# Performance work log

Hardware: AMD Instinct MI355X
Metric: run time of the kernel (lower is better)

## Reference

```python
import jax, jax.numpy as jnp
import numpy as np

N = 2048            # num nodes
AVG_DEG = 16
E0 = N * AVG_DEG    # random edges; self-loops appended -> E = E0 + N
IN_FEATS = 256
H = 16              # num_heads
HS = 32             # hidden_size (forced by linear001 = Linear(32,16))
D = HS // H         # head_dim = 2
EPS = 1e-5


def gat_conv(x, src, dst, W, al, ar, b):
    # DGL-style GATConv: x [N,F] -> [N,H,D]
    feat = (x @ W).reshape(N, H, D)                      # [N,H,D]
    el = (feat * al[None]).sum(-1)                       # [N,H] (src term)
    er = (feat * ar[None]).sum(-1)                       # [N,H] (dst term)
    e = jax.nn.leaky_relu(el[src] + er[dst], 0.2)        # [E,H]
    m = jax.ops.segment_max(e, dst, num_segments=N)      # segment softmax over incoming edges
    ex = jnp.exp(e - m[dst])
    s = jax.ops.segment_sum(ex, dst, num_segments=N)
    alpha = ex / s[dst]                                  # [E,H]
    out = jax.ops.segment_sum(alpha[:, :, None] * feat[src], dst, num_segments=N)
    return out + b.reshape(1, H, D)


def setup_inputs() -> dict:
    key = jax.random.key(0)
    ks = jax.random.split(key, 40)
    rn = lambda k, s, sc=0.1: (jax.random.normal(k, s, jnp.float32) * sc)
    loops = jnp.arange(N, dtype=jnp.int32)
    src = jnp.concatenate([jax.random.randint(ks[0], (E0,), 0, N, jnp.int32), loops])
    dst = jnp.concatenate([jax.random.randint(ks[1], (E0,), 0, N, jnp.int32), loops])
    inp = {
        'features': jax.random.normal(ks[2], (N, IN_FEATS), jnp.float32),
        'src': src, 'dst': dst,
        # GATConv 1
        'W1': rn(ks[3], (IN_FEATS, HS)), 'al1': rn(ks[4], (H, D)), 'ar1': rn(ks[5], (H, D)), 'bg1': rn(ks[6], (HS,)),
        # GATConv 2
        'W2': rn(ks[7], (HS, HS)), 'al2': rn(ks[8], (H, D)), 'ar2': rn(ks[9], (H, D)), 'bg2': rn(ks[10], (HS,)),
        # dense MHA projections
        'qw': rn(ks[11], (HS, HS)), 'qb': rn(ks[12], (HS,)),
        'kw': rn(ks[13], (HS, HS)), 'kb': rn(ks[14], (HS,)),
        'vw': rn(ks[15], (HS, HS)), 'vb': rn(ks[16], (HS,)),
        'ow': rn(ks[17], (HS, HS)), 'ob': rn(ks[18], (HS,)),
        # batchnorm affine
        'bn_g': jnp.ones((HS,), jnp.float32), 'bn_b': jnp.zeros((HS,), jnp.float32),
        # mlp
        'm1w': rn(ks[19], (HS, HS // 2)), 'm1b': rn(ks[20], (HS // 2,)),
        'm2w': rn(ks[21], (HS // 2, HS)), 'm2b': rn(ks[22], (HS,)),
        # scoring head
        'w001': rn(ks[23], (32, 16)), 'b001': rn(ks[24], (16,)),
        'w01': rn(ks[25], (16, 8)), 'b01': rn(ks[26], (8,)),
        'w1': rn(ks[27], (8, 4)), 'b1': rn(ks[28], (4,)),
        'w2': rn(ks[29], (4, 1)), 'b2': rn(ks[30], (1,)),
    }
    return inp


def reference(features, src, dst, W1, al1, ar1, bg1, W2, al2, ar2, bg2,
              qw, qb, kw, kb, vw, vb, ow, ob, bn_g, bn_b,
              m1w, m1b, m2w, m2b, w001, b001, w01, b01, w1, b1, w2, b2):
    h = gat_conv(features, src, dst, W1, al1, ar1, bg1).reshape(N, HS)
    h = gat_conv(h, src, dst, W2, al2, ar2, bg2).reshape(N, HS)
    # manual dense multi-head attention across all nodes
    Q = (h @ qw + qb).reshape(N, H, D)
    K = (h @ kw + kb).reshape(N, H, D)
    V = (h @ vw + vb).reshape(N, H, D)
    scores = jnp.einsum('nhd,mhd->hnm', Q, K) / jnp.sqrt(jnp.float32(D))  # [H,N,N]
    attn = jax.nn.softmax(scores, axis=-1)
    ao = jnp.einsum('hnm,mhd->nhd', attn, V).reshape(N, HS)
    ao = ao @ ow + ob
    # BatchNorm1d (training mode: batch stats, biased variance)
    mu = ao.mean(0)
    var = ao.var(0)
    ao = (ao - mu) / jnp.sqrt(var + EPS) * bn_g + bn_b
    # MLP
    ao = jax.nn.relu(ao @ m1w + m1b)
    ao = jax.nn.relu(ao @ m2w + m2b)
    # scoring head
    z = jax.nn.leaky_relu(ao @ w001 + b001, 0.01)
    z = jax.nn.leaky_relu(z @ w01 + b01, 0.01)
    z = jax.nn.leaky_relu(z @ w1 + b1, 0.01)
    return jax.nn.sigmoid(z @ w2 + b2)  # [N,1]
```

## Files before the change

kernel.cpp:

```cpp
#include <hip/hip_runtime.h>
#include <math.h>

#define NN 2048
#define NH 16
#define HSZ 32
#define INF_ 256
#define CAP 64

__global__ void __launch_bounds__(256) k_front(
    const float* __restrict__ x, const float* __restrict__ W1,
    const float* __restrict__ al, const float* __restrict__ ar,
    const int* __restrict__ src, const int* __restrict__ dst, int E,
    int* __restrict__ cnt, int* __restrict__ adj, float* __restrict__ feat,
    float* __restrict__ el, float* __restrict__ er) {
    __shared__ float xs[4][INF_];
    __shared__ float row[4][HSZ];
    const int tid = threadIdx.x;
    const int gtid = blockIdx.x * 256 + tid;
    const int lane = tid & 63, wsl = tid >> 6, gw = gtid >> 6;
    const int j = lane & 31, half = lane >> 5;

    if (gtid < E) {
        int d = dst[gtid];
        int pos = atomicAdd(&cnt[d], 1);
        if (pos < CAP) adj[d * CAP + pos] = src[gtid];
    }

    int n = gw;
    ((float4*)xs[wsl])[lane] = ((const float4*)(x + (size_t)n * INF_))[lane];
    __syncthreads();
    float acc = 0.f;
    const float4* x4 = (const float4*)xs[wsl];
#pragma unroll
    for (int k4 = 0; k4 < 32; ++k4) {
        float4 xq = x4[half * 32 + k4];
        int k = half * 128 + 4 * k4;
        acc += xq.x * W1[(k + 0) * HSZ + j];
        acc += xq.y * W1[(k + 1) * HSZ + j];
        acc += xq.z * W1[(k + 2) * HSZ + j];
        acc += xq.w * W1[(k + 3) * HSZ + j];
    }
    acc += __shfl_xor(acc, 32);
    if (half == 0) {
        feat[n * HSZ + j] = acc;
        row[wsl][j] = acc;
    }
    __syncthreads();
    if (lane < NH) {
        el[n * NH + lane] =
            row[wsl][2 * lane] * al[2 * lane] + row[wsl][2 * lane + 1] * al[2 * lane + 1];
    } else if (lane < 2 * NH) {
        int h = lane - NH;
        er[n * NH + h] =
            row[wsl][2 * h] * ar[2 * h] + row[wsl][2 * h + 1] * ar[2 * h + 1];
    }
}

__global__ void __launch_bounds__(256) k_seg_gat2(
    const int* __restrict__ cnt, const int* __restrict__ adj,
    const float* __restrict__ el, const float* __restrict__ er,
    const float* __restrict__ feat, const float* __restrict__ bg,
    const float* __restrict__ W2, const float* __restrict__ al2,
    const float* __restrict__ ar2, float* __restrict__ feat2,
    float* __restrict__ el2, float* __restrict__ er2) {
    __shared__ float row[4][HSZ];
    __shared__ float xv[4][HSZ];
    const int tid = threadIdx.x;
    const int gtid = blockIdx.x * 256 + tid;
    const int lane = tid & 63, wsl = tid >> 6, gw = gtid >> 6;
    const int j = lane & 31, half = lane >> 5;
    int n = gw;
    int h = lane >> 2, q = lane & 3;
    int deg = cnt[n]; deg = deg < CAP ? deg : CAP;
    int base = n * CAP;
    float erv = er[n * NH + h];
    float sum = 0.f, a0 = 0.f, a1 = 0.f;
    for (int jj = q; jj < deg; jj += 4) {
        int s = adj[base + jj];
        float v = el[s * NH + h] + erv;
        v = v > 0.f ? v : 0.2f * v;
        float ex = __expf(v);
        float2 f = ((const float2*)feat)[s * NH + h];
        sum += ex; a0 += ex * f.x; a1 += ex * f.y;
    }
    sum += __shfl_xor(sum, 1); a0 += __shfl_xor(a0, 1); a1 += __shfl_xor(a1, 1);
    sum += __shfl_xor(sum, 2); a0 += __shfl_xor(a0, 2); a1 += __shfl_xor(a1, 2);
    if (q == 0) {
        float rs = 1.f / sum;
        row[wsl][2 * h]     = a0 * rs + bg[2 * h];
        row[wsl][2 * h + 1] = a1 * rs + bg[2 * h + 1];
    }
    __syncthreads();
    float acc = 0.f;
#pragma unroll
    for (int c = half * 16; c < half * 16 + 16; ++c) acc += row[wsl][c] * W2[c * HSZ + j];
    acc += __shfl_xor(acc, 32);
    if (half == 0) {
        feat2[n * HSZ + j] = acc;
        xv[wsl][j] = acc;
    }
    __syncthreads();
    if (lane < NH) {
        el2[n * NH + lane] =
            xv[wsl][2 * lane] * al2[2 * lane] + xv[wsl][2 * lane + 1] * al2[2 * lane + 1];
    } else if (lane < 2 * NH) {
        int h2 = lane - NH;
        er2[n * NH + h2] =
            xv[wsl][2 * h2] * ar2[2 * h2] + xv[wsl][2 * h2 + 1] * ar2[2 * h2 + 1];
    }
}

__global__ void __launch_bounds__(256) k_seg_qkv(
    const int* __restrict__ cnt, const int* __restrict__ adj,
    const float* __restrict__ el2, const float* __restrict__ er2,
    const float* __restrict__ feat2, const float* __restrict__ bg,
    const float* __restrict__ qw, const float* __restrict__ qb,
    const float* __restrict__ kw, const float* __restrict__ kb,
    const float* __restrict__ vw, const float* __restrict__ vb,
    float* __restrict__ Q, float* __restrict__ Kt, float* __restrict__ Vt) {
    __shared__ float row[4][HSZ];
    const int tid = threadIdx.x;
    const int gtid = blockIdx.x * 256 + tid;
    const int lane = tid & 63, wsl = tid >> 6, gw = gtid >> 6;
    const int j = lane & 31, half = lane >> 5;
    int n = gw;
    int h = lane >> 2, q = lane & 3;
    int deg = cnt[n]; deg = deg < CAP ? deg : CAP;
    int base = n * CAP;
    float erv = er2[n * NH + h];
    float sum = 0.f, a0 = 0.f, a1 = 0.f;
    for (int jj = q; jj < deg; jj += 4) {
        int s = adj[base + jj];
        float v = el2[s * NH + h] + erv;
        v = v > 0.f ? v : 0.2f * v;
        float ex = __expf(v);
        float2 f = ((const float2*)feat2)[s * NH + h];
        sum += ex; a0 += ex * f.x; a1 += ex * f.y;
    }
    sum += __shfl_xor(sum, 1); a0 += __shfl_xor(a0, 1); a1 += __shfl_xor(a1, 1);
    sum += __shfl_xor(sum, 2); a0 += __shfl_xor(a0, 2); a1 += __shfl_xor(a1, 2);
    if (q == 0) {
        float rs = 1.f / sum;
        row[wsl][2 * h]     = a0 * rs + bg[2 * h];
        row[wsl][2 * h + 1] = a1 * rs + bg[2 * h + 1];
    }
    __syncthreads();
    float qa = 0.f, ka = 0.f, va = 0.f;
#pragma unroll
    for (int c = half * 16; c < half * 16 + 16; ++c) {
        float hv = row[wsl][c];
        qa += hv * qw[c * HSZ + j];
        ka += hv * kw[c * HSZ + j];
        va += hv * vw[c * HSZ + j];
    }
    qa += __shfl_xor(qa, 32);
    ka += __shfl_xor(ka, 32);
    va += __shfl_xor(va, 32);
    if (half == 0) {
        const float QS = 0.70710678118654752f * 1.44269504088896340f;
        Q[n * HSZ + j] = (qa + qb[j]) * QS;
        int hh = j >> 1, d = j & 1;
        Kt[hh * (NN * 2) + n * 2 + d] = ka + kb[j];
        Vt[hh * (NN * 2) + n * 2 + d] = va + vb[j];
    }
}

__global__ void __launch_bounds__(256) k_attn16(
    const float* __restrict__ Q, const float* __restrict__ Kt,
    const float* __restrict__ Vt, float* __restrict__ ao) {
    const int gtid = blockIdx.x * 256 + threadIdx.x;
    const int gw = gtid >> 6;
    const int lane = gtid & 63;
    int hh = gw >> 7;
    int q0 = (gw & 127) * 16;
    const float2* K2 = (const float2*)Kt + hh * NN;
    const float2* V2 = (const float2*)Vt + hh * NN;
    float qx[16], qy[16], sm[16], a0[16], a1[16];
#pragma unroll
    for (int i = 0; i < 16; ++i) {
        float2 qq = ((const float2*)Q)[(q0 + i) * NH + hh];
        qx[i] = qq.x; qy[i] = qq.y;
        sm[i] = 0.f; a0[i] = 0.f; a1[i] = 0.f;
    }
#pragma unroll 2
    for (int it = 0; it < NN / 64; ++it) {
        float2 kk = K2[it * 64 + lane];
        float2 vv = V2[it * 64 + lane];
#pragma unroll
        for (int i = 0; i < 16; ++i) {
            float pe = exp2f(qx[i] * kk.x + qy[i] * kk.y);
            sm[i] += pe; a0[i] += pe * vv.x; a1[i] += pe * vv.y;
        }
    }
#pragma unroll
    for (int i = 0; i < 16; ++i) {
#pragma unroll
        for (int off = 32; off; off >>= 1) {
            sm[i] += __shfl_xor(sm[i], off);
            a0[i] += __shfl_xor(a0[i], off);
            a1[i] += __shfl_xor(a1[i], off);
        }
        if (lane == 0) {
            float rs = 1.f / sm[i];
            ((float2*)ao)[(q0 + i) * NH + hh] = make_float2(a0[i] * rs, a1[i] * rs);
        }
    }
}

__global__ void __launch_bounds__(256) k_oproj(
    const float* __restrict__ ao, const float* __restrict__ ow,
    const float* __restrict__ ob, float* __restrict__ X,
    float* __restrict__ bnbuf) {
    __shared__ float as[256];
    __shared__ float xv[256];
    int tid = threadIdx.x;
    int row0 = blockIdx.x * 8;
    as[tid] = ao[row0 * HSZ + tid];
    __syncthreads();
    int r = tid >> 5, j = tid & 31;
    float a = ob[j];
#pragma unroll
    for (int c = 0; c < HSZ; ++c) a += as[r * HSZ + c] * ow[c * HSZ + j];
    X[(row0 + r) * HSZ + j] = a;
    xv[tid] = a;
    __syncthreads();
    if (tid < HSZ) {
        float s = 0.f, q = 0.f;
#pragma unroll
        for (int rr = 0; rr < 8; ++rr) {
            float v = xv[rr * HSZ + tid];
            s += v;
            q += v * v;
        }
        atomicAdd(&bnbuf[tid], s);
        atomicAdd(&bnbuf[HSZ + tid], q);
    }
}

#define M1W 0
#define M2W 512
#define W001 1024
#define W01 1536
#define W1O 1664
#define W2O 1696
#define M1B 1700
#define M2B 1716
#define B001 1748
#define B01 1764
#define B1O 1772
#define B2O 1776
#define AO 1780
#define BO 1812
__global__ void __launch_bounds__(64) k_tail(
    const float* __restrict__ X, const float* __restrict__ bnbuf,
    const float* __restrict__ bn_g, const float* __restrict__ bn_b,
    const float* __restrict__ m1w, const float* __restrict__ m1b,
    const float* __restrict__ m2w, const float* __restrict__ m2b,
    const float* __restrict__ w001, const float* __restrict__ b001,
    const float* __restrict__ w01, const float* __restrict__ b01,
    const float* __restrict__ w1, const float* __restrict__ b1,
    const float* __restrict__ w2, const float* __restrict__ b2,
    float* __restrict__ out) {
    __shared__ float w_s[1844];
    __shared__ float xb[16][33];
    __shared__ float yb[16][17];
    __shared__ float zb[16][33];
    __shared__ float ab[16][17];
    __shared__ float bb[16][9];
    __shared__ float cb[16][5];
    const int t = threadIdx.x;
#pragma unroll
    for (int i = 0; i < 8; ++i) {
        int idx = t + i * 64;
        w_s[M1W + idx] = m1w[idx];
        w_s[M2W + idx] = m2w[idx];
        w_s[W001 + idx] = w001[idx];
    }
    w_s[W01 + t] = w01[t];
    w_s[W01 + 64 + t] = w01[64 + t];
    if (t < 32) {
        w_s[W1O + t] = w1[t];
        w_s[M2B + t] = m2b[t];
        const float invN = 1.f / NN;
        float mu = bnbuf[t] * invN;
        float var = bnbuf[HSZ + t] * invN - mu * mu;
        float A = rsqrtf(var + 1e-5f) * bn_g[t];
        w_s[AO + t] = A;
        w_s[BO + t] = bn_b[t] - mu * A;
    }
    if (t < 16) { w_s[M1B + t] = m1b[t]; w_s[B001 + t] = b001[t]; }
    if (t < 8) w_s[B01 + t] = b01[t];
    if (t < 4) { w_s[B1O + t] = b1[t]; w_s[W2O + t] = w2[t]; }
    if (t == 0) w_s[B2O] = b2[0];
    __syncthreads();

    const int nl = t >> 2, sub = t & 3;
    const int n = blockIdx.x * 16 + nl;

    {
        const float4* X4 = (const float4*)(X + n * HSZ + sub * 8);
        float4 v0 = X4[0], v1 = X4[1];
        int i0 = sub * 8;
        xb[nl][i0 + 0] = v0.x * w_s[AO + i0 + 0] + w_s[BO + i0 + 0];
        xb[nl][i0 + 1] = v0.y * w_s[AO + i0 + 1] + w_s[BO + i0 + 1];
        xb[nl][i0 + 2] = v0.z * w_s[AO + i0 + 2] + w_s[BO + i0 + 2];
        xb[nl][i0 + 3] = v0.w * w_s[AO + i0 + 3] + w_s[BO + i0 + 3];
        xb[nl][i0 + 4] = v1.x * w_s[AO + i0 + 4] + w_s[BO + i0 + 4];
        xb[nl][i0 + 5] = v1.y * w_s[AO + i0 + 5] + w_s[BO + i0 + 5];
        xb[nl][i0 + 6] = v1.z * w_s[AO + i0 + 6] + w_s[BO + i0 + 6];
        xb[nl][i0 + 7] = v1.w * w_s[AO + i0 + 7] + w_s[BO + i0 + 7];
    }
    __syncthreads();
    {
        int jj0 = sub * 4;
        float acc0 = w_s[M1B + jj0], acc1 = w_s[M1B + jj0 + 1];
        float acc2 = w_s[M1B + jj0 + 2], acc3 = w_s[M1B + jj0 + 3];
#pragma unroll
        for (int i = 0; i < 32; ++i) {
            float xv = xb[nl][i];
            acc0 += xv * w_s[M1W + i * 16 + jj0 + 0];
            acc1 += xv * w_s[M1W + i * 16 + jj0 + 1];
            acc2 += xv * w_s[M1W + i * 16 + jj0 + 2];
            acc3 += xv * w_s[M1W + i * 16 + jj0 + 3];
        }
        yb[nl][jj0 + 0] = fmaxf(acc0, 0.f);
        yb[nl][jj0 + 1] = fmaxf(acc1, 0.f);
        yb[nl][jj0 + 2] = fmaxf(acc2, 0.f);
        yb[nl][jj0 + 3] = fmaxf(acc3, 0.f);
    }
    __syncthreads();
    {
        int jj0 = sub * 8;
        float acc[8];
#pragma unroll
        for (int k = 0; k < 8; ++k) acc[k] = w_s[M2B + jj0 + k];
#pragma unroll
        for (int i = 0; i < 16; ++i) {
            float yv = yb[nl][i];
#pragma unroll
            for (int k = 0; k < 8; ++k) acc[k] += yv * w_s[M2W + i * 32 + jj0 + k];
        }
#pragma unroll
        for (int k = 0; k < 8; ++k) zb[nl][jj0 + k] = fmaxf(acc[k], 0.f);
    }
    __syncthreads();
    {
        int jj0 = sub * 4;
        float acc0 = w_s[B001 + jj0], acc1 = w_s[B001 + jj0 + 1];
        float acc2 = w_s[B001 + jj0 + 2], acc3 = w_s[B001 + jj0 + 3];
#pragma unroll
        for (int i = 0; i < 32; ++i) {
            float zv = zb[nl][i];
            acc0 += zv * w_s[W001 + i * 16 + jj0 + 0];
            acc1 += zv * w_s[W001 + i * 16 + jj0 + 1];
            acc2 += zv * w_s[W001 + i * 16 + jj0 + 2];
            acc3 += zv * w_s[W001 + i * 16 + jj0 + 3];
        }
        ab[nl][jj0 + 0] = acc0 > 0.f ? acc0 : 0.01f * acc0;
        ab[nl][jj0 + 1] = acc1 > 0.f ? acc1 : 0.01f * acc1;
        ab[nl][jj0 + 2] = acc2 > 0.f ? acc2 : 0.01f * acc2;
        ab[nl][jj0 + 3] = acc3 > 0.f ? acc3 : 0.01f * acc3;
    }
    __syncthreads();
    {
        int jj0 = sub * 2;
        float acc0 = w_s[B01 + jj0], acc1 = w_s[B01 + jj0 + 1];
#pragma unroll
        for (int i = 0; i < 16; ++i) {
            float av = ab[nl][i];
            acc0 += av * w_s[W01 + i * 8 + jj0 + 0];
            acc1 += av * w_s[W01 + i * 8 + jj0 + 1];
        }
        bb[nl][jj0 + 0] = acc0 > 0.f ? acc0 : 0.01f * acc0;
        bb[nl][jj0 + 1] = acc1 > 0.f ? acc1 : 0.01f * acc1;
    }
    __syncthreads();
    {
        float acc = w_s[B1O + sub];
#pragma unroll
        for (int i = 0; i < 8; ++i) acc += bb[nl][i] * w_s[W1O + i * 4 + sub];
        cb[nl][sub] = acc > 0.f ? acc : 0.01f * acc;
    }
    __syncthreads();
    if (sub == 0) {
        float d = w_s[B2O];
#pragma unroll
        for (int i = 0; i < 4; ++i) d += cb[nl][i] * w_s[W2O + i];
        out[n] = 1.f / (1.f + __expf(-d));
    }
}

extern "C" void kernel_launch(void* const* d_in, const int* in_sizes, int n_in,
                              void* d_out, int out_size, void* d_ws, size_t ws_size,
                              hipStream_t stream) {
    const float* features = (const float*)d_in[0];
    const int* src = (const int*)d_in[1];
    const int* dst = (const int*)d_in[2];
    const float* W1 = (const float*)d_in[3];
    const float* al1 = (const float*)d_in[4];
    const float* ar1 = (const float*)d_in[5];
    const float* bg1 = (const float*)d_in[6];
    const float* W2 = (const float*)d_in[7];
    const float* al2 = (const float*)d_in[8];
    const float* ar2 = (const float*)d_in[9];
    const float* bg2 = (const float*)d_in[10];
    const float* qw = (const float*)d_in[11];
    const float* qb = (const float*)d_in[12];
    const float* kw = (const float*)d_in[13];
    const float* kb = (const float*)d_in[14];
    const float* vw = (const float*)d_in[15];
    const float* vb = (const float*)d_in[16];
    const float* ow = (const float*)d_in[17];
    const float* ob = (const float*)d_in[18];
    const float* bn_g = (const float*)d_in[19];
    const float* bn_b = (const float*)d_in[20];
    const float* m1w = (const float*)d_in[21];
    const float* m1b = (const float*)d_in[22];
    const float* m2w = (const float*)d_in[23];
    const float* m2b = (const float*)d_in[24];
    const float* w001 = (const float*)d_in[25];
    const float* b001 = (const float*)d_in[26];
    const float* w01 = (const float*)d_in[27];
    const float* b01 = (const float*)d_in[28];
    const float* w1 = (const float*)d_in[29];
    const float* b1 = (const float*)d_in[30];
    const float* w2 = (const float*)d_in[31];
    const float* b2 = (const float*)d_in[32];

    int E = in_sizes[1];

    float* wsp = (float*)d_ws;
    float* feat = wsp;
    float* el = feat + NN * HSZ;
    float* er = el + NN * NH;
    float* feat2 = er + NN * NH;
    float* el2 = feat2 + NN * HSZ;
    float* er2 = el2 + NN * NH;
    float* Q = er2 + NN * NH;
    float* Kt = Q + NN * HSZ;
    float* Vt = Kt + NN * HSZ;
    float* ao = Vt + NN * HSZ;
    float* X = ao + NN * HSZ;
    float* bnbuf = X + NN * HSZ;
    int* cnt = (int*)(bnbuf + 64);
    int* adj = cnt + NN;

    dim3 b256(256);
    hipMemsetAsync(bnbuf, 0, (64 + NN) * sizeof(float), stream);

    k_front<<<512, b256, 0, stream>>>(features, W1, al1, ar1, src, dst, E,
                                      cnt, adj, feat, el, er);
    k_seg_gat2<<<512, b256, 0, stream>>>(cnt, adj, el, er, feat, bg1,
                                         W2, al2, ar2, feat2, el2, er2);
    k_seg_qkv<<<512, b256, 0, stream>>>(cnt, adj, el2, er2, feat2, bg2,
                                        qw, qb, kw, kb, vw, vb, Q, Kt, Vt);
    k_attn16<<<512, b256, 0, stream>>>(Q, Kt, Vt, ao);
    k_oproj<<<256, b256, 0, stream>>>(ao, ow, ob, X, bnbuf);
    k_tail<<<128, dim3(64), 0, stream>>>(X, bnbuf, bn_g, bn_b, m1w, m1b, m2w, m2b,
                                         w001, b001, w01, b01, w1, b1, w2, b2,
                                         (float*)d_out);
}
```

Before: 189.4 us.

## Fuse dense attention with output projection and interleave K/V into float4

Merges the all-pairs attention kernel and the output-projection/batchnorm-stats kernel into one. Each block now handles 8 nodes across all 16 heads, with each wave looping over 4 heads. The per-node attention output stays in shared memory instead of making a round trip through global memory, and one launch is removed. K and V are stored interleaved per head so each key step is a single float4 load. The trade-off is that each loaded key is reused across only 8 queries instead of 16, and the grid has half as many waves, which lowers occupancy in the exp-heavy loop.

```diff
diff --git a/kernel.cpp b/kernel.cpp
--- a/kernel.cpp
+++ b/kernel.cpp
@@ -117,7 +117,7 @@
     const float* __restrict__ qw, const float* __restrict__ qb,
     const float* __restrict__ kw, const float* __restrict__ kb,
     const float* __restrict__ vw, const float* __restrict__ vb,
-    float* __restrict__ Q, float* __restrict__ Kt, float* __restrict__ Vt) {
+    float* __restrict__ Q, float* __restrict__ KV) {
     __shared__ float row[4][HSZ];
     const int tid = threadIdx.x;
     const int gtid = blockIdx.x * 256 + tid;
@@ -160,80 +160,70 @@
         const float QS = 0.70710678118654752f * 1.44269504088896340f;
         Q[n * HSZ + j] = (qa + qb[j]) * QS;
         int hh = j >> 1, d = j & 1;
-        Kt[hh * (NN * 2) + n * 2 + d] = ka + kb[j];
-        Vt[hh * (NN * 2) + n * 2 + d] = va + vb[j];
-    }
-}
-
-__global__ void __launch_bounds__(256) k_attn16(
-    const float* __restrict__ Q, const float* __restrict__ Kt,
-    const float* __restrict__ Vt, float* __restrict__ ao) {
-    const int gtid = blockIdx.x * 256 + threadIdx.x;
-    const int gw = gtid >> 6;
-    const int lane = gtid & 63;
-    int hh = gw >> 7;
-    int q0 = (gw & 127) * 16;
-    const float2* K2 = (const float2*)Kt + hh * NN;
-    const float2* V2 = (const float2*)Vt + hh * NN;
-    float qx[16], qy[16], sm[16], a0[16], a1[16];
-#pragma unroll
-    for (int i = 0; i < 16; ++i) {
-        float2 qq = ((const float2*)Q)[(q0 + i) * NH + hh];
-        qx[i] = qq.x; qy[i] = qq.y;
-        sm[i] = 0.f; a0[i] = 0.f; a1[i] = 0.f;
-    }
+        KV[(hh * NN + n) * 4 + d]     = ka + kb[j];
+        KV[(hh * NN + n) * 4 + 2 + d] = va + vb[j];
+    }
+}
+
+__global__ void __launch_bounds__(256) k_attn_op(
+    const float* __restrict__ Q, const float* __restrict__ KV,
+    const float* __restrict__ ow, const float* __restrict__ ob,
+    float* __restrict__ X, float* __restrict__ bnbuf) {
+    __shared__ float ao_s[8][34];
+    __shared__ float xs2[8][34];
+    const int tid = threadIdx.x;
+    const int lane = tid & 63, wsl = tid >> 6;
+    const int n0 = blockIdx.x * 8;
+    const float4* KV4 = (const float4*)KV;
+    const float2* Q2 = (const float2*)Q;
+#pragma unroll 1
+    for (int p = 0; p < 4; ++p) {
+        const int hh = wsl * 4 + p;
+        float qx[8], qy[8], sm[8], a0[8], a1[8];
+#pragma unroll
+        for (int i = 0; i < 8; ++i) {
+            float2 qq = Q2[(n0 + i) * NH + hh];
+            qx[i] = qq.x; qy[i] = qq.y;
+            sm[i] = 0.f; a0[i] = 0.f; a1[i] = 0.f;
+        }
 #pragma unroll 2
-    for (int it = 0; it < NN / 64; ++it) {
-        float2 kk = K2[it * 64 + lane];
-        float2 vv = V2[it * 64 + lane];
-#pragma unroll
-        for (int i = 0; i < 16; ++i) {
-            float pe = exp2f(qx[i] * kk.x + qy[i] * kk.y);
-            sm[i] += pe; a0[i] += pe * vv.x; a1[i] += pe * vv.y;
-        }
-    }
-#pragma unroll
-    for (int i = 0; i < 16; ++i) {
-#pragma unroll
-        for (int off = 32; off; off >>= 1) {
-            sm[i] += __shfl_xor(sm[i], off);
-            a0[i] += __shfl_xor(a0[i], off);
-            a1[i] += __shfl_xor(a1[i], off);
-        }
-        if (lane == 0) {
-            float rs = 1.f / sm[i];
-            ((float2*)ao)[(q0 + i) * NH + hh] = make_float2(a0[i] * rs, a1[i] * rs);
-        }
-    }
-}
-
-__global__ void __launch_bounds__(256) k_oproj(
-    const float* __restrict__ ao, const float* __restrict__ ow,
-    const float* __restrict__ ob, float* __restrict__ X,
-    float* __restrict__ bnbuf) {
-    __shared__ float as[256];
-    __shared__ float xv[256];
-    int tid = threadIdx.x;
-    int row0 = blockIdx.x * 8;
-    as[tid] = ao[row0 * HSZ + tid];
-    __syncthreads();
-    int r = tid >> 5, j = tid & 31;
+        for (int it = 0; it < NN / 64; ++it) {
+            float4 kv = KV4[hh * NN + it * 64 + lane];
+#pragma unroll
+            for (int i = 0; i < 8; ++i) {
+                float pe = exp2f(qx[i] * kv.x + qy[i] * kv.y);
+                sm[i] += pe; a0[i] += pe * kv.z; a1[i] += pe * kv.w;
+            }
+        }
+#pragma unroll
+        for (int i = 0; i < 8; ++i) {
+#pragma unroll
+            for (int off = 32; off; off >>= 1) {
+                sm[i] += __shfl_xor(sm[i], off);
+                a0[i] += __shfl_xor(a0[i], off);
+                a1[i] += __shfl_xor(a1[i], off);
+            }
+            if (lane == 0) {
+                float rs = 1.f / sm[i];
+                ao_s[i][2 * hh]     = a0[i] * rs;
+                ao_s[i][2 * hh + 1] = a1[i] * rs;
+            }
+        }
+    }
+    __syncthreads();
+    const int nl = tid >> 5, j = tid & 31;
     float a = ob[j];
 #pragma unroll
-    for (int c = 0; c < HSZ; ++c) a += as[r * HSZ + c] * ow[c * HSZ + j];
-    X[(row0 + r) * HSZ + j] = a;
-    xv[tid] = a;
+    for (int c = 0; c < HSZ; ++c) a += ao_s[nl][c] * ow[c * HSZ + j];
+    X[(n0 + nl) * HSZ + j] = a;
+    xs2[nl][j] = a;
     __syncthreads();
     if (tid < HSZ) {
-        float s = 0.f, q = 0.f;
-#pragma unroll
-        for (int rr = 0; rr < 8; ++rr) {
-            float v = xv[rr * HSZ + tid];
-            s += v;
-            q += v * v;
-        }
+        float s = 0.f, qsum = 0.f;
+#pragma unroll
+        for (int r = 0; r < 8; ++r) { float v = xs2[r][tid]; s += v; qsum += v * v; }
         atomicAdd(&bnbuf[tid], s);
-        atomicAdd(&bnbuf[HSZ + tid], q);
+        atomicAdd(&bnbuf[HSZ + tid], qsum);
     }
 }
 
@@ -437,9 +427,8 @@
     float* el2 = feat2 + NN * HSZ;
     float* er2 = el2 + NN * NH;
     float* Q = er2 + NN * NH;
-    float* Kt = Q + NN * HSZ;
-    float* Vt = Kt + NN * HSZ;
-    float* ao = Vt + NN * HSZ;
+    float* KV = Q + NN * HSZ;
+    float* ao = KV + NN * HSZ * 2;
     float* X = ao + NN * HSZ;
     float* bnbuf = X + NN * HSZ;
     int* cnt = (int*)(bnbuf + 64);
@@ -453,9 +442,8 @@
     k_seg_gat2<<<512, b256, 0, stream>>>(cnt, adj, el, er, feat, bg1,
                                          W2, al2, ar2, feat2, el2, er2);
     k_seg_qkv<<<512, b256, 0, stream>>>(cnt, adj, el2, er2, feat2, bg2,
-                                        qw, qb, kw, kb, vw, vb, Q, Kt, Vt);
-    k_attn16<<<512, b256, 0, stream>>>(Q, Kt, Vt, ao);
-    k_oproj<<<256, b256, 0, stream>>>(ao, ow, ob, X, bnbuf);
+                                        qw, qb, kw, kb, vw, vb, Q, KV);
+    k_attn_op<<<256, b256, 0, stream>>>(Q, KV, ow, ob, X, bnbuf);
     k_tail<<<128, dim3(64), 0, stream>>>(X, bnbuf, bn_g, bn_b, m1w, m1b, m2w, m2b,
                                          w001, b001, w01, b01, w1, b1, w2, b2,
                                          (float*)d_out);
```

Result: slower. 195.5 us (+3.2%).
